# Kernel tuning notes

Measured on AMD Instinct MI355X. Metric: run time of the kernel, lower is better.

## Reference

```python
import jax, jax.numpy as jnp
import numpy as np

B, S, D, H = 2, 2048, 1024, 16
DK = D // H


def setup_inputs() -> dict:
    key = jax.random.key(0)
    ks = jax.random.split(key, 12)
    scale = 1.0 / np.sqrt(D)
    inp = {
        "Q": jax.random.normal(ks[0], (B, S, D), jnp.float32),
        "K": jax.random.normal(ks[1], (B, S, D), jnp.float32),
        "V": jax.random.normal(ks[2], (B, S, D), jnp.float32),
        # causal mask, broadcastable to [B, H, S, S]; 0 -> masked
        "Mask": jnp.tril(jnp.ones((S, S), jnp.int32))[None, None],
        "Wq": jax.random.normal(ks[3], (D, D), jnp.float32) * scale,
        "bq": jnp.zeros((D,), jnp.float32),
        "Wk": jax.random.normal(ks[4], (D, D), jnp.float32) * scale,
        "bk": jnp.zeros((D,), jnp.float32),
        "Wv": jax.random.normal(ks[5], (D, D), jnp.float32) * scale,
        "bv": jnp.zeros((D,), jnp.float32),
        "Wo": jax.random.normal(ks[6], (D, D), jnp.float32) * scale,
        "bo": jnp.zeros((D,), jnp.float32),
    }
    return inp


def _heads(x):
    # [B, S, D] -> [B, H, S, DK]
    return x.reshape(B, S, H, DK).transpose(0, 2, 1, 3)


def reference(Q, K, V, Mask, Wq, bq, Wk, bk, Wv, bv, Wo, bo):
    q = _heads(Q @ Wq.T + bq)
    k = _heads(K @ Wk.T + bk)
    v = _heads(V @ Wv.T + bv)
    # NOTE: original module does NOT scale by 1/sqrt(d_k)
    logits = jnp.einsum("bhqd,bhkd->bhqk", q, k)
    logits = jnp.where(Mask == 0, jnp.float32(-1e9), logits)
    attn = jax.nn.softmax(logits, axis=-1)  # dropout p=0.0 -> identity
    ctx = jnp.einsum("bhqk,bhkd->bhqd", attn, v)
    ctx = ctx.transpose(0, 2, 1, 3).reshape(B, S, D)
    return ctx @ Wo.T + bo
```

## Files before the change

kernel.cpp:

```cpp
#include <hip/hip_runtime.h>
#include <hip/hip_bf16.h>

#define B_  2
#define S_  2048
#define D_  1024
#define H_  16
#define DK_ 64
#define M_  (B_ * S_)

typedef __bf16 bf16;
typedef __bf16 bf16x8 __attribute__((ext_vector_type(8)));
typedef __bf16 bf16x4 __attribute__((ext_vector_type(4)));
typedef float  f32x4  __attribute__((ext_vector_type(4)));

#define MFMA16(a, b, c) __builtin_amdgcn_mfma_f32_16x16x32_bf16((a), (b), (c), 0, 0, 0)

__device__ __forceinline__ void gl2lds16(const bf16* g, bf16* l) {
    __builtin_amdgcn_global_load_lds((const __attribute__((address_space(1))) void*)g,
                                     (__attribute__((address_space(3))) void*)l, 16, 0, 0);
}

struct CastArgs { const float* src[7]; bf16* dst[7]; };

__global__ __launch_bounds__(256) void cast_all(CastArgs a) {
    int i = blockIdx.x * 256 + threadIdx.x;
    int seg, off;
    if (i < 3145728) { seg = i >> 20; off = i & 1048575; }
    else { int j = i - 3145728; seg = 3 + (j >> 18); off = j & 262143; }
    float4 v = ((const float4*)a.src[seg])[off];
    bf16x4 o;
    o[0] = (bf16)v.x; o[1] = (bf16)v.y; o[2] = (bf16)v.z; o[3] = (bf16)v.w;
    *(bf16x4*)&a.dst[seg][(size_t)off * 4] = o;
}

struct QkvArgs { const bf16* A[3]; const bf16* W[3]; const float* bias[3]; bf16* out[3]; };

__global__ __launch_bounds__(256, 3) void gemm_qkv(QkvArgs ar) {
    __shared__ bf16 As[128 * 32];
    __shared__ bf16 Bs[128 * 32];

    const int z = blockIdx.z;
    const bf16* A  = ar.A[z];
    const bf16* Bt = ar.W[z];
    const float* bias = ar.bias[z];
    bf16* Out = ar.out[z];
    const int mode = (z == 2) ? 1 : 0;

    const int t = threadIdx.x, lane = t & 63, w = t >> 6;
    const int lr = lane & 15, lq = lane >> 4;
    const int wm = (w >> 1) * 64, wn = (w & 1) * 64;
    const int n0 = blockIdx.x * 128, m0 = blockIdx.y * 128;

    const int c0 = w * 128 + lane, c1 = c0 + 64;
    const bf16* Ag0 = A  + (size_t)(m0 + (c0 >> 2)) * 1024 + (c0 & 3) * 8;
    const bf16* Ag1 = A  + (size_t)(m0 + (c1 >> 2)) * 1024 + (c1 & 3) * 8;
    const bf16* Bg0 = Bt + (size_t)(n0 + (c0 >> 2)) * 1024 + (c0 & 3) * 8;
    const bf16* Bg1 = Bt + (size_t)(n0 + (c1 >> 2)) * 1024 + (c1 & 3) * 8;
    bf16* Al0 = As + (w * 128) * 8;
    bf16* Al1 = As + (w * 128 + 64) * 8;
    bf16* Bl0 = Bs + (w * 128) * 8;
    bf16* Bl1 = Bs + (w * 128 + 64) * 8;

    f32x4 acc[4][4];
#pragma unroll
    for (int mi = 0; mi < 4; ++mi)
#pragma unroll
        for (int ni = 0; ni < 4; ++ni) acc[mi][ni] = 0.0f;

    for (int k0 = 0; k0 < 1024; k0 += 32) {
        __syncthreads();
        gl2lds16(Ag0 + k0, Al0);
        gl2lds16(Ag1 + k0, Al1);
        gl2lds16(Bg0 + k0, Bl0);
        gl2lds16(Bg1 + k0, Bl1);
        __syncthreads();
        bf16x8 af[4], bfr[4];
#pragma unroll
        for (int mi = 0; mi < 4; ++mi) af[mi]  = *(const bf16x8*)&As[(wm + mi * 16 + lr) * 32 + lq * 8];
#pragma unroll
        for (int ni = 0; ni < 4; ++ni) bfr[ni] = *(const bf16x8*)&Bs[(wn + ni * 16 + lr) * 32 + lq * 8];
#pragma unroll
        for (int mi = 0; mi < 4; ++mi)
#pragma unroll
            for (int ni = 0; ni < 4; ++ni) acc[mi][ni] = MFMA16(af[mi], bfr[ni], acc[mi][ni]);
    }

#pragma unroll
    for (int mi = 0; mi < 4; ++mi) {
#pragma unroll
        for (int ni = 0; ni < 4; ++ni) {
            int gn = n0 + wn + ni * 16 + lr;
            float bv = bias[gn];
#pragma unroll
            for (int r = 0; r < 4; ++r) {
                int gm = m0 + wm + mi * 16 + lq * 4 + r;
                float v = acc[mi][ni][r] + bv;
                int b = gm >> 11, s = gm & (S_ - 1);
                int h = gn >> 6, dk = gn & 63;
                if (mode == 0)
                    Out[(((size_t)(b * H_ + h) * S_ + s) << 6) + dk] = (bf16)v;
                else
                    Out[(((size_t)(b * H_ + h) * DK_ + dk) << 11) + s] = (bf16)v;
            }
        }
    }
}

__global__ __launch_bounds__(256, 2) void gemm_out(const bf16* __restrict__ A,
                                                   const bf16* __restrict__ Bt,
                                                   const float* __restrict__ bias,
                                                   float* __restrict__ Out) {
    __shared__ bf16 As[64 * 32];
    __shared__ bf16 Bs[128 * 32];

    const int t = threadIdx.x, lane = t & 63, w = t >> 6;
    const int lr = lane & 15, lq = lane >> 4;
    const int wm = (w >> 1) * 32, wn = (w & 1) * 64;
    const int n0 = blockIdx.x * 128, m0 = blockIdx.y * 64;

    const int ca = w * 64 + lane;
    const int cb0 = w * 128 + lane, cb1 = cb0 + 64;
    const bf16* Ag  = A  + (size_t)(m0 + (ca >> 2)) * 1024 + (ca & 3) * 8;
    const bf16* Bg0 = Bt + (size_t)(n0 + (cb0 >> 2)) * 1024 + (cb0 & 3) * 8;
    const bf16* Bg1 = Bt + (size_t)(n0 + (cb1 >> 2)) * 1024 + (cb1 & 3) * 8;
    bf16* Al  = As + (w * 64) * 8;
    bf16* Bl0 = Bs + (w * 128) * 8;
    bf16* Bl1 = Bs + (w * 128 + 64) * 8;

    f32x4 acc[2][4];
#pragma unroll
    for (int mi = 0; mi < 2; ++mi)
#pragma unroll
        for (int ni = 0; ni < 4; ++ni) acc[mi][ni] = 0.0f;

    for (int k0 = 0; k0 < 1024; k0 += 32) {
        __syncthreads();
        gl2lds16(Ag + k0, Al);
        gl2lds16(Bg0 + k0, Bl0);
        gl2lds16(Bg1 + k0, Bl1);
        __syncthreads();
        bf16x8 af[2], bfr[4];
#pragma unroll
        for (int mi = 0; mi < 2; ++mi) af[mi]  = *(const bf16x8*)&As[(wm + mi * 16 + lr) * 32 + lq * 8];
#pragma unroll
        for (int ni = 0; ni < 4; ++ni) bfr[ni] = *(const bf16x8*)&Bs[(wn + ni * 16 + lr) * 32 + lq * 8];
#pragma unroll
        for (int mi = 0; mi < 2; ++mi)
#pragma unroll
            for (int ni = 0; ni < 4; ++ni) acc[mi][ni] = MFMA16(af[mi], bfr[ni], acc[mi][ni]);
    }

#pragma unroll
    for (int mi = 0; mi < 2; ++mi) {
#pragma unroll
        for (int ni = 0; ni < 4; ++ni) {
            int gn = n0 + wn + ni * 16 + lr;
            float bv = bias[gn];
#pragma unroll
            for (int r = 0; r < 4; ++r) {
                int gm = m0 + wm + mi * 16 + lq * 4 + r;
                Out[(size_t)gm * 1024 + gn] = acc[mi][ni][r] + bv;
            }
        }
    }
}

__global__ __launch_bounds__(256, 2) void flash_attn(const bf16* __restrict__ qh,
                                                     const bf16* __restrict__ kh,
                                                     const bf16* __restrict__ vt,
                                                     bf16* __restrict__ ctx) {
    __shared__ char smem[40960];
    bf16* Qs = (bf16*)smem;
    bf16* Ks = (bf16*)(smem + 8192);
    bf16* Ps = (bf16*)(smem + 24576);

    const int pair = blockIdx.x, h = blockIdx.y, b = blockIdx.z;
    const int bh = b * H_ + h;
    const bf16* Qp = qh + (size_t)bh * S_ * DK_;
    const bf16* Kp = kh + (size_t)bh * S_ * DK_;
    const bf16* Vp = vt + (size_t)bh * DK_ * S_;

    const int t = threadIdx.x, lane = t & 63, w = t >> 6;
    const int lr = lane & 15, lq = lane >> 4;
    const int wq = w & 1, wk = w >> 1;
    bf16* Pw = Ps + w * 2048;

    for (int half = 0; half < 2; ++half) {
        const int qt = half ? (31 - pair) : pair;

#pragma unroll
        for (int i = 0; i < 2; ++i) {
            int c = w * 128 + i * 64 + lane;
            int qrow = c >> 3, xx = (c & 7) ^ (qrow & 7);
            gl2lds16(Qp + (size_t)(qt * 64 + qrow) * 64 + xx * 8, Qs + (w * 128 + i * 64) * 8);
        }

        f32x4 oacc[2][4];
#pragma unroll
        for (int mt = 0; mt < 2; ++mt)
#pragma unroll
            for (int nt = 0; nt < 4; ++nt) oacc[mt][nt] = 0.0f;
        float lpart[2] = {0.f, 0.f};

        const int nkt = qt / 2 + 1;
        for (int kt = 0; kt < nkt; ++kt) {
            __syncthreads();
#pragma unroll
            for (int i = 0; i < 4; ++i) {
                int c = w * 256 + i * 64 + lane;
                int krow = c >> 3, xx = (c & 7) ^ (krow & 7);
                gl2lds16(Kp + (size_t)(kt * 128 + krow) * 64 + xx * 8, Ks + (w * 256 + i * 64) * 8);
            }
            __syncthreads();

            const int k64 = kt * 2 + wk;
            if (k64 <= qt) {
                bf16x8 bv[2][4];
#pragma unroll
                for (int kk = 0; kk < 2; ++kk)
#pragma unroll
                    for (int nt = 0; nt < 4; ++nt)
                        bv[kk][nt] = *(const bf16x8*)(Vp + (size_t)(nt * 16 + lr) * S_ +
                                                      kt * 128 + wk * 64 + kk * 32 + lq * 8);
                f32x4 s[4][2];
#pragma unroll
                for (int mt = 0; mt < 4; ++mt)
#pragma unroll
                    for (int nt = 0; nt < 2; ++nt) s[mt][nt] = 0.0f;
#pragma unroll
                for (int ks = 0; ks < 2; ++ks) {
                    bf16x8 af[4], qf[2];
                    int xx = (ks * 4 + lq) ^ (lr & 7);
#pragma unroll
                    for (int mt = 0; mt < 4; ++mt)
                        af[mt] = *(const bf16x8*)&Ks[(wk * 64 + mt * 16 + lr) * 64 + xx * 8];
#pragma unroll
                    for (int nt = 0; nt < 2; ++nt)
                        qf[nt] = *(const bf16x8*)&Qs[(wq * 32 + nt * 16 + lr) * 64 + xx * 8];
#pragma unroll
                    for (int mt = 0; mt < 4; ++mt)
#pragma unroll
                        for (int nt = 0; nt < 2; ++nt) s[mt][nt] = MFMA16(af[mt], qf[nt], s[mt][nt]);
                }
                const bool diag = (k64 == qt);
#pragma unroll
                for (int mt = 0; mt < 4; ++mt)
#pragma unroll
                    for (int nt = 0; nt < 2; ++nt) {
                        bf16x4 pb;
#pragma unroll
                        for (int r = 0; r < 4; ++r) {
                            int kl = mt * 16 + lq * 4 + r;
                            int qlT = wq * 32 + nt * 16 + lr;
                            float p = (!diag || kl <= qlT) ? __expf(s[mt][nt][r]) : 0.0f;
                            bf16 p16 = (bf16)p;
                            lpart[nt] += (float)p16;
                            pb[r] = p16;
                        }
                        int xx = (2 * mt + (lq >> 1)) ^ (lr & 7);
                        *(bf16x4*)&Pw[(nt * 16 + lr) * 64 + xx * 8 + (lq & 1) * 4] = pb;
                    }
#pragma unroll
                for (int kk = 0; kk < 2; ++kk) {
                    bf16x8 ap[2];
                    int xx = (kk * 4 + lq) ^ (lr & 7);
#pragma unroll
                    for (int mt2 = 0; mt2 < 2; ++mt2)
                        ap[mt2] = *(const bf16x8*)&Pw[(mt2 * 16 + lr) * 64 + xx * 8];
#pragma unroll
                    for (int mt2 = 0; mt2 < 2; ++mt2)
#pragma unroll
                        for (int nt = 0; nt < 4; ++nt)
                            oacc[mt2][nt] = MFMA16(ap[mt2], bv[kk][nt], oacc[mt2][nt]);
                }
            }
        }

        __syncthreads();
#pragma unroll
        for (int nt = 0; nt < 2; ++nt) {
            lpart[nt] += __shfl_xor(lpart[nt], 16);
            lpart[nt] += __shfl_xor(lpart[nt], 32);
        }
        float* Op = (float*)(smem + 24576);
        float* Lh = (float*)smem;
        if (lq == 0)
#pragma unroll
            for (int nt = 0; nt < 2; ++nt) Lh[wk * 64 + wq * 32 + nt * 16 + lr] = lpart[nt];
        if (wk == 1) {
#pragma unroll
            for (int mt = 0; mt < 2; ++mt)
#pragma unroll
                for (int nt = 0; nt < 4; ++nt)
#pragma unroll
                    for (int r = 0; r < 4; ++r) {
                        int row = mt * 16 + lq * 4 + r, col = nt * 16 + lr;
                        int xx = (col >> 2) ^ (row & 15);
                        Op[wq * 2048 + row * 64 + xx * 4 + (col & 3)] = oacc[mt][nt][r];
                    }
        }
        __syncthreads();
        if (wk == 0) {
            float linv[2][4];
#pragma unroll
            for (int mt = 0; mt < 2; ++mt)
#pragma unroll
                for (int r = 0; r < 4; ++r) {
                    int qq = wq * 32 + mt * 16 + lq * 4 + r;
                    linv[mt][r] = 1.0f / (Lh[qq] + Lh[64 + qq]);
                }
#pragma unroll
            for (int mt = 0; mt < 2; ++mt)
#pragma unroll
                for (int nt = 0; nt < 4; ++nt)
#pragma unroll
                    for (int r = 0; r < 4; ++r) {
                        int row = mt * 16 + lq * 4 + r, col = nt * 16 + lr;
                        int xx = (col >> 2) ^ (row & 15);
                        float v = (oacc[mt][nt][r] + Op[wq * 2048 + row * 64 + xx * 4 + (col & 3)]) * linv[mt][r];
                        int q = qt * 64 + wq * 32 + row;
                        ctx[((size_t)(b * S_ + q)) * D_ + h * DK_ + col] = (bf16)v;
                    }
        }
        __syncthreads();
    }
}

extern "C" void kernel_launch(void* const* d_in, const int* in_sizes, int n_in,
                              void* d_out, int out_size, void* d_ws, size_t ws_size,
                              hipStream_t stream) {
    const float* Q  = (const float*)d_in[0];
    const float* K  = (const float*)d_in[1];
    const float* V  = (const float*)d_in[2];
    const float* Wq = (const float*)d_in[4];
    const float* bq = (const float*)d_in[5];
    const float* Wk = (const float*)d_in[6];
    const float* bk = (const float*)d_in[7];
    const float* Wv = (const float*)d_in[8];
    const float* bv = (const float*)d_in[9];
    const float* Wo = (const float*)d_in[10];
    const float* bo = (const float*)d_in[11];

    char* p = (char*)d_ws;
    bf16* Qb  = (bf16*)p;  p += (size_t)M_ * D_ * 2;
    bf16* Kb  = (bf16*)p;  p += (size_t)M_ * D_ * 2;
    bf16* Vb  = (bf16*)p;  p += (size_t)M_ * D_ * 2;
    bf16* Wqb = (bf16*)p;  p += (size_t)D_ * D_ * 2;
    bf16* Wkb = (bf16*)p;  p += (size_t)D_ * D_ * 2;
    bf16* Wvb = (bf16*)p;  p += (size_t)D_ * D_ * 2;
    bf16* Wob = (bf16*)p;  p += (size_t)D_ * D_ * 2;
    bf16* qhd = (bf16*)p;  p += (size_t)M_ * D_ * 2;
    bf16* khd = (bf16*)p;  p += (size_t)M_ * D_ * 2;
    bf16* vtr = (bf16*)p;  p += (size_t)M_ * D_ * 2;
    bf16* ctx = (bf16*)p;  p += (size_t)M_ * D_ * 2;

    CastArgs ca;
    ca.src[0] = Q;  ca.dst[0] = Qb;
    ca.src[1] = K;  ca.dst[1] = Kb;
    ca.src[2] = V;  ca.dst[2] = Vb;
    ca.src[3] = Wq; ca.dst[3] = Wqb;
    ca.src[4] = Wk; ca.dst[4] = Wkb;
    ca.src[5] = Wv; ca.dst[5] = Wvb;
    ca.src[6] = Wo; ca.dst[6] = Wob;
    cast_all<<<16384, 256, 0, stream>>>(ca);

    QkvArgs qa;
    qa.A[0] = Qb;  qa.A[1] = Kb;  qa.A[2] = Vb;
    qa.W[0] = Wqb; qa.W[1] = Wkb; qa.W[2] = Wvb;
    qa.bias[0] = bq; qa.bias[1] = bk; qa.bias[2] = bv;
    qa.out[0] = qhd; qa.out[1] = khd; qa.out[2] = vtr;
    dim3 qgrid(D_ / 128, M_ / 128, 3);
    gemm_qkv<<<qgrid, 256, 0, stream>>>(qa);

    dim3 fgrid(16, H_, B_);
    flash_attn<<<fgrid, 256, 0, stream>>>(qhd, khd, vtr, ctx);

    dim3 ogrid(D_ / 128, M_ / 64);
    gemm_out<<<ogrid, 256, 0, stream>>>(ctx, Wob, bo, (float*)d_out);
}
```

Before: 240.6 us.

## Shrink attention query tile to 32 rows and stage V-transpose stores through LDS

The flash attention kernel now processes 32-query tiles, with each of four waves handling a 32-key slice. This doubles the grid to 1024 blocks with a swizzled block-to-head mapping, cuts LDS use, and raises the occupancy hint to 4 blocks. The partial outputs and row sums of the four waves are reduced through LDS at the end. Separately, the QKV GEMM's transposed V output is staged in a padded LDS tile so it can be written with 16-byte coalesced stores instead of scattered 2-byte writes. The price is extra LDS traffic and a larger shared-memory footprint in the GEMM, which may lower its occupancy.

```diff
diff --git a/kernel.cpp b/kernel.cpp
--- a/kernel.cpp
+++ b/kernel.cpp
@@ -38,6 +38,7 @@
 __global__ __launch_bounds__(256, 3) void gemm_qkv(QkvArgs ar) {
     __shared__ bf16 As[128 * 32];
     __shared__ bf16 Bs[128 * 32];
+    __shared__ bf16 Cs[128 * 136];
 
     const int z = blockIdx.z;
     const bf16* A  = ar.A[z];
@@ -85,23 +86,45 @@
             for (int ni = 0; ni < 4; ++ni) acc[mi][ni] = MFMA16(af[mi], bfr[ni], acc[mi][ni]);
     }
 
-#pragma unroll
-    for (int mi = 0; mi < 4; ++mi) {
-#pragma unroll
-        for (int ni = 0; ni < 4; ++ni) {
-            int gn = n0 + wn + ni * 16 + lr;
-            float bv = bias[gn];
-#pragma unroll
-            for (int r = 0; r < 4; ++r) {
-                int gm = m0 + wm + mi * 16 + lq * 4 + r;
-                float v = acc[mi][ni][r] + bv;
-                int b = gm >> 11, s = gm & (S_ - 1);
-                int h = gn >> 6, dk = gn & 63;
-                if (mode == 0)
+    if (mode == 0) {
+#pragma unroll
+        for (int mi = 0; mi < 4; ++mi) {
+#pragma unroll
+            for (int ni = 0; ni < 4; ++ni) {
+                int gn = n0 + wn + ni * 16 + lr;
+                float bv = bias[gn];
+#pragma unroll
+                for (int r = 0; r < 4; ++r) {
+                    int gm = m0 + wm + mi * 16 + lq * 4 + r;
+                    float v = acc[mi][ni][r] + bv;
+                    int b = gm >> 11, s = gm & (S_ - 1);
+                    int h = gn >> 6, dk = gn & 63;
                     Out[(((size_t)(b * H_ + h) * S_ + s) << 6) + dk] = (bf16)v;
-                else
-                    Out[(((size_t)(b * H_ + h) * DK_ + dk) << 11) + s] = (bf16)v;
+                }
             }
+        }
+    } else {
+#pragma unroll
+        for (int mi = 0; mi < 4; ++mi) {
+#pragma unroll
+            for (int ni = 0; ni < 4; ++ni) {
+                int n = wn + ni * 16 + lr;
+                float bv = bias[n0 + n];
+                bf16x4 pk;
+#pragma unroll
+                for (int r = 0; r < 4; ++r) pk[r] = (bf16)(acc[mi][ni][r] + bv);
+                *(bf16x4*)&Cs[n * 136 + wm + mi * 16 + lq * 4] = pk;
+            }
+        }
+        __syncthreads();
+        const int b = m0 >> 11, s0 = m0 & (S_ - 1);
+#pragma unroll
+        for (int j = 0; j < 8; ++j) {
+            int cc = j * 256 + t;
+            int n = cc >> 4, cm = cc & 15;
+            int gn = n0 + n, h = gn >> 6, dk = gn & 63;
+            bf16x8 v = *(const bf16x8*)&Cs[n * 136 + cm * 8];
+            *(bf16x8*)&Out[(((size_t)(b * H_ + h) * DK_ + dk) << 11) + s0 + cm * 8] = v;
         }
     }
 }
@@ -165,34 +188,35 @@
     }
 }
 
-__global__ __launch_bounds__(256, 2) void flash_attn(const bf16* __restrict__ qh,
+__global__ __launch_bounds__(256, 4) void flash_attn(const bf16* __restrict__ qh,
                                                      const bf16* __restrict__ kh,
                                                      const bf16* __restrict__ vt,
                                                      bf16* __restrict__ ctx) {
-    __shared__ char smem[40960];
+    __shared__ char smem[30720];
     bf16* Qs = (bf16*)smem;
-    bf16* Ks = (bf16*)(smem + 8192);
-    bf16* Ps = (bf16*)(smem + 24576);
-
-    const int pair = blockIdx.x, h = blockIdx.y, b = blockIdx.z;
-    const int bh = b * H_ + h;
+    bf16* Ks = (bf16*)(smem + 4096);
+    bf16* Ps = (bf16*)(smem + 20480);
+
+    const int id = blockIdx.x;
+    const int bh = (id & 7) * 4 + ((id >> 3) & 3);
+    const int pr = id >> 5;
+    const int b = bh >> 4, h = bh & 15;
+
     const bf16* Qp = qh + (size_t)bh * S_ * DK_;
     const bf16* Kp = kh + (size_t)bh * S_ * DK_;
     const bf16* Vp = vt + (size_t)bh * DK_ * S_;
 
     const int t = threadIdx.x, lane = t & 63, w = t >> 6;
     const int lr = lane & 15, lq = lane >> 4;
-    const int wq = w & 1, wk = w >> 1;
-    bf16* Pw = Ps + w * 2048;
+    bf16* Pw = Ps + w * (32 * 40);
 
     for (int half = 0; half < 2; ++half) {
-        const int qt = half ? (31 - pair) : pair;
-
-#pragma unroll
-        for (int i = 0; i < 2; ++i) {
-            int c = w * 128 + i * 64 + lane;
+        const int qt = half ? (63 - pr) : pr;
+
+        {
+            int c = w * 64 + lane;
             int qrow = c >> 3, xx = (c & 7) ^ (qrow & 7);
-            gl2lds16(Qp + (size_t)(qt * 64 + qrow) * 64 + xx * 8, Qs + (w * 128 + i * 64) * 8);
+            gl2lds16(Qp + (size_t)(qt * 32 + qrow) * 64 + xx * 8, Qs + (w * 64) * 8);
         }
 
         f32x4 oacc[2][4];
@@ -202,7 +226,7 @@
             for (int nt = 0; nt < 4; ++nt) oacc[mt][nt] = 0.0f;
         float lpart[2] = {0.f, 0.f};
 
-        const int nkt = qt / 2 + 1;
+        const int nkt = (qt >> 2) + 1;
         for (int kt = 0; kt < nkt; ++kt) {
             __syncthreads();
 #pragma unroll
@@ -213,66 +237,64 @@
             }
             __syncthreads();
 
-            const int k64 = kt * 2 + wk;
-            if (k64 <= qt) {
-                bf16x8 bv[2][4];
-#pragma unroll
-                for (int kk = 0; kk < 2; ++kk)
-#pragma unroll
-                    for (int nt = 0; nt < 4; ++nt)
-                        bv[kk][nt] = *(const bf16x8*)(Vp + (size_t)(nt * 16 + lr) * S_ +
-                                                      kt * 128 + wk * 64 + kk * 32 + lq * 8);
-                f32x4 s[4][2];
-#pragma unroll
-                for (int mt = 0; mt < 4; ++mt)
+            const int k32 = kt * 4 + w;
+            if (k32 <= qt) {
+                bf16x8 bv[4];
+#pragma unroll
+                for (int nt = 0; nt < 4; ++nt)
+                    bv[nt] = *(const bf16x8*)(Vp + (size_t)(nt * 16 + lr) * S_ +
+                                              kt * 128 + w * 32 + lq * 8);
+                f32x4 s[2][2];
+#pragma unroll
+                for (int mt = 0; mt < 2; ++mt)
 #pragma unroll
                     for (int nt = 0; nt < 2; ++nt) s[mt][nt] = 0.0f;
 #pragma unroll
                 for (int ks = 0; ks < 2; ++ks) {
-                    bf16x8 af[4], qf[2];
-                    int xx = (ks * 4 + lq) ^ (lr & 7);
-#pragma unroll
-                    for (int mt = 0; mt < 4; ++mt)
-                        af[mt] = *(const bf16x8*)&Ks[(wk * 64 + mt * 16 + lr) * 64 + xx * 8];
-#pragma unroll
-                    for (int nt = 0; nt < 2; ++nt)
-                        qf[nt] = *(const bf16x8*)&Qs[(wq * 32 + nt * 16 + lr) * 64 + xx * 8];
-#pragma unroll
-                    for (int mt = 0; mt < 4; ++mt)
+                    bf16x8 af[2], qf[2];
+#pragma unroll
+                    for (int mt = 0; mt < 2; ++mt) {
+                        int krow = w * 32 + mt * 16 + lr;
+                        int xx = (ks * 4 + lq) ^ (krow & 7);
+                        af[mt] = *(const bf16x8*)&Ks[krow * 64 + xx * 8];
+                    }
+#pragma unroll
+                    for (int nt = 0; nt < 2; ++nt) {
+                        int q = nt * 16 + lr;
+                        int xx = (ks * 4 + lq) ^ (q & 7);
+                        qf[nt] = *(const bf16x8*)&Qs[q * 64 + xx * 8];
+                    }
+#pragma unroll
+                    for (int mt = 0; mt < 2; ++mt)
 #pragma unroll
                         for (int nt = 0; nt < 2; ++nt) s[mt][nt] = MFMA16(af[mt], qf[nt], s[mt][nt]);
                 }
-                const bool diag = (k64 == qt);
-#pragma unroll
-                for (int mt = 0; mt < 4; ++mt)
+                const bool diag = (k32 == qt);
+#pragma unroll
+                for (int mt = 0; mt < 2; ++mt)
 #pragma unroll
                     for (int nt = 0; nt < 2; ++nt) {
                         bf16x4 pb;
 #pragma unroll
                         for (int r = 0; r < 4; ++r) {
                             int kl = mt * 16 + lq * 4 + r;
-                            int qlT = wq * 32 + nt * 16 + lr;
-                            float p = (!diag || kl <= qlT) ? __expf(s[mt][nt][r]) : 0.0f;
+                            int ql = nt * 16 + lr;
+                            float p = (!diag || kl <= ql) ? __expf(s[mt][nt][r]) : 0.0f;
                             bf16 p16 = (bf16)p;
                             lpart[nt] += (float)p16;
                             pb[r] = p16;
                         }
-                        int xx = (2 * mt + (lq >> 1)) ^ (lr & 7);
-                        *(bf16x4*)&Pw[(nt * 16 + lr) * 64 + xx * 8 + (lq & 1) * 4] = pb;
+                        *(bf16x4*)&Pw[(nt * 16 + lr) * 40 + mt * 16 + lq * 4] = pb;
                     }
-#pragma unroll
-                for (int kk = 0; kk < 2; ++kk) {
-                    bf16x8 ap[2];
-                    int xx = (kk * 4 + lq) ^ (lr & 7);
-#pragma unroll
-                    for (int mt2 = 0; mt2 < 2; ++mt2)
-                        ap[mt2] = *(const bf16x8*)&Pw[(mt2 * 16 + lr) * 64 + xx * 8];
-#pragma unroll
-                    for (int mt2 = 0; mt2 < 2; ++mt2)
-#pragma unroll
-                        for (int nt = 0; nt < 4; ++nt)
-                            oacc[mt2][nt] = MFMA16(ap[mt2], bv[kk][nt], oacc[mt2][nt]);
-                }
+                bf16x8 ap[2];
+#pragma unroll
+                for (int mt2 = 0; mt2 < 2; ++mt2)
+                    ap[mt2] = *(const bf16x8*)&Pw[(mt2 * 16 + lr) * 40 + lq * 8];
+#pragma unroll
+                for (int mt2 = 0; mt2 < 2; ++mt2)
+#pragma unroll
+                    for (int nt = 0; nt < 4; ++nt)
+                        oacc[mt2][nt] = MFMA16(ap[mt2], bv[nt], oacc[mt2][nt]);
             }
         }
 
@@ -282,32 +304,31 @@
             lpart[nt] += __shfl_xor(lpart[nt], 16);
             lpart[nt] += __shfl_xor(lpart[nt], 32);
         }
-        float* Op = (float*)(smem + 24576);
-        float* Lh = (float*)smem;
+        float* Op = (float*)smem;
+        float* Lh = (float*)(smem + 26112);
         if (lq == 0)
 #pragma unroll
-            for (int nt = 0; nt < 2; ++nt) Lh[wk * 64 + wq * 32 + nt * 16 + lr] = lpart[nt];
-        if (wk == 1) {
+            for (int nt = 0; nt < 2; ++nt) Lh[w * 32 + nt * 16 + lr] = lpart[nt];
+        if (w > 0) {
 #pragma unroll
             for (int mt = 0; mt < 2; ++mt)
 #pragma unroll
                 for (int nt = 0; nt < 4; ++nt)
 #pragma unroll
                     for (int r = 0; r < 4; ++r) {
-                        int row = mt * 16 + lq * 4 + r, col = nt * 16 + lr;
-                        int xx = (col >> 2) ^ (row & 15);
-                        Op[wq * 2048 + row * 64 + xx * 4 + (col & 3)] = oacc[mt][nt][r];
+                        int q = mt * 16 + lq * 4 + r, dk = nt * 16 + lr;
+                        Op[(w - 1) * 2176 + q * 68 + dk] = oacc[mt][nt][r];
                     }
         }
         __syncthreads();
-        if (wk == 0) {
+        if (w == 0) {
             float linv[2][4];
 #pragma unroll
             for (int mt = 0; mt < 2; ++mt)
 #pragma unroll
                 for (int r = 0; r < 4; ++r) {
-                    int qq = wq * 32 + mt * 16 + lq * 4 + r;
-                    linv[mt][r] = 1.0f / (Lh[qq] + Lh[64 + qq]);
+                    int q = mt * 16 + lq * 4 + r;
+                    linv[mt][r] = 1.0f / (Lh[q] + Lh[32 + q] + Lh[64 + q] + Lh[96 + q]);
                 }
 #pragma unroll
             for (int mt = 0; mt < 2; ++mt)
@@ -315,11 +336,12 @@
                 for (int nt = 0; nt < 4; ++nt)
 #pragma unroll
                     for (int r = 0; r < 4; ++r) {
-                        int row = mt * 16 + lq * 4 + r, col = nt * 16 + lr;
-                        int xx = (col >> 2) ^ (row & 15);
-                        float v = (oacc[mt][nt][r] + Op[wq * 2048 + row * 64 + xx * 4 + (col & 3)]) * linv[mt][r];
-                        int q = qt * 64 + wq * 32 + row;
-                        ctx[((size_t)(b * S_ + q)) * D_ + h * DK_ + col] = (bf16)v;
+                        int q = mt * 16 + lq * 4 + r, dk = nt * 16 + lr;
+                        float v = oacc[mt][nt][r] + Op[q * 68 + dk]
+                                + Op[2176 + q * 68 + dk] + Op[4352 + q * 68 + dk];
+                        v *= linv[mt][r];
+                        int qg = qt * 32 + q;
+                        ctx[((size_t)(b * S_ + qg)) * D_ + h * DK_ + dk] = (bf16)v;
                     }
         }
         __syncthreads();
@@ -372,8 +394,7 @@
     dim3 qgrid(D_ / 128, M_ / 128, 3);
     gemm_qkv<<<qgrid, 256, 0, stream>>>(qa);
 
-    dim3 fgrid(16, H_, B_);
-    flash_attn<<<fgrid, 256, 0, stream>>>(qhd, khd, vtr, ctx);
+    flash_attn<<<1024, 256, 0, stream>>>(qhd, khd, vtr, ctx);
 
     dim3 ogrid(D_ / 128, M_ / 64);
     gemm_out<<<ogrid, 256, 0, stream>>>(ctx, Wob, bo, (float*)d_out);
```

New measurement: 241.6 us. Within noise of the previous version (+0.4%).

## Deepen GEMM K-tiles with swizzled LDS, stage V-transpose store, remap attention blocks to XCDs

Applied to the files above, without the earlier changes.

Both projection GEMMs now load a 64-wide K slice per iteration into XOR-swizzled LDS tiles, halving the number of barrier pairs and avoiding bank conflicts on fragment reads. The transposed V output goes through an LDS staging buffer so global stores become contiguous 16-byte writes instead of scattered 2-byte writes. Flash attention uses a 1D grid whose block index is remapped so that all blocks for a given batch-head land on the same XCD, improving L2 reuse of K/V. Larger LDS footprints may reduce occupancy.

```diff
diff --git a/kernel.cpp b/kernel.cpp
--- a/kernel.cpp
+++ b/kernel.cpp
@@ -36,8 +36,10 @@
 struct QkvArgs { const bf16* A[3]; const bf16* W[3]; const float* bias[3]; bf16* out[3]; };
 
 __global__ __launch_bounds__(256, 3) void gemm_qkv(QkvArgs ar) {
-    __shared__ bf16 As[128 * 32];
-    __shared__ bf16 Bs[128 * 32];
+    __shared__ char smem[34816];
+    bf16* As = (bf16*)smem;
+    bf16* Bs = (bf16*)(smem + 16384);
+    bf16* Cs = (bf16*)smem;
 
     const int z = blockIdx.z;
     const bf16* A  = ar.A[z];
@@ -51,15 +53,16 @@
     const int wm = (w >> 1) * 64, wn = (w & 1) * 64;
     const int n0 = blockIdx.x * 128, m0 = blockIdx.y * 128;
 
-    const int c0 = w * 128 + lane, c1 = c0 + 64;
-    const bf16* Ag0 = A  + (size_t)(m0 + (c0 >> 2)) * 1024 + (c0 & 3) * 8;
-    const bf16* Ag1 = A  + (size_t)(m0 + (c1 >> 2)) * 1024 + (c1 & 3) * 8;
-    const bf16* Bg0 = Bt + (size_t)(n0 + (c0 >> 2)) * 1024 + (c0 & 3) * 8;
-    const bf16* Bg1 = Bt + (size_t)(n0 + (c1 >> 2)) * 1024 + (c1 & 3) * 8;
-    bf16* Al0 = As + (w * 128) * 8;
-    bf16* Al1 = As + (w * 128 + 64) * 8;
-    bf16* Bl0 = Bs + (w * 128) * 8;
-    bf16* Bl1 = Bs + (w * 128 + 64) * 8;
+    const bf16* Ag[4]; const bf16* Bg[4]; bf16* Al[4]; bf16* Bl[4];
+#pragma unroll
+    for (int i = 0; i < 4; ++i) {
+        int c = i * 256 + w * 64 + lane;
+        int row = c >> 3, x = (c & 7) ^ (row & 7);
+        Ag[i] = A  + (size_t)(m0 + row) * 1024 + x * 8;
+        Bg[i] = Bt + (size_t)(n0 + row) * 1024 + x * 8;
+        Al[i] = As + (i * 256 + w * 64) * 8;
+        Bl[i] = Bs + (i * 256 + w * 64) * 8;
+    }
 
     f32x4 acc[4][4];
 #pragma unroll
@@ -67,41 +70,74 @@
 #pragma unroll
         for (int ni = 0; ni < 4; ++ni) acc[mi][ni] = 0.0f;
 
-    for (int k0 = 0; k0 < 1024; k0 += 32) {
-        __syncthreads();
-        gl2lds16(Ag0 + k0, Al0);
-        gl2lds16(Ag1 + k0, Al1);
-        gl2lds16(Bg0 + k0, Bl0);
-        gl2lds16(Bg1 + k0, Bl1);
-        __syncthreads();
-        bf16x8 af[4], bfr[4];
-#pragma unroll
-        for (int mi = 0; mi < 4; ++mi) af[mi]  = *(const bf16x8*)&As[(wm + mi * 16 + lr) * 32 + lq * 8];
-#pragma unroll
-        for (int ni = 0; ni < 4; ++ni) bfr[ni] = *(const bf16x8*)&Bs[(wn + ni * 16 + lr) * 32 + lq * 8];
-#pragma unroll
-        for (int mi = 0; mi < 4; ++mi)
-#pragma unroll
-            for (int ni = 0; ni < 4; ++ni) acc[mi][ni] = MFMA16(af[mi], bfr[ni], acc[mi][ni]);
-    }
-
-#pragma unroll
-    for (int mi = 0; mi < 4; ++mi) {
-#pragma unroll
-        for (int ni = 0; ni < 4; ++ni) {
-            int gn = n0 + wn + ni * 16 + lr;
-            float bv = bias[gn];
-#pragma unroll
-            for (int r = 0; r < 4; ++r) {
-                int gm = m0 + wm + mi * 16 + lq * 4 + r;
-                float v = acc[mi][ni][r] + bv;
-                int b = gm >> 11, s = gm & (S_ - 1);
-                int h = gn >> 6, dk = gn & 63;
-                if (mode == 0)
+    for (int k0 = 0; k0 < 1024; k0 += 64) {
+        __syncthreads();
+#pragma unroll
+        for (int i = 0; i < 4; ++i) {
+            gl2lds16(Ag[i] + k0, Al[i]);
+            gl2lds16(Bg[i] + k0, Bl[i]);
+        }
+        __syncthreads();
+#pragma unroll
+        for (int ks = 0; ks < 2; ++ks) {
+            bf16x8 af[4], bfr[4];
+#pragma unroll
+            for (int mi = 0; mi < 4; ++mi) {
+                int row = wm + mi * 16 + lr;
+                af[mi] = *(const bf16x8*)&As[row * 64 + ((ks * 4 + lq) ^ (row & 7)) * 8];
+            }
+#pragma unroll
+            for (int ni = 0; ni < 4; ++ni) {
+                int row = wn + ni * 16 + lr;
+                bfr[ni] = *(const bf16x8*)&Bs[row * 64 + ((ks * 4 + lq) ^ (row & 7)) * 8];
+            }
+#pragma unroll
+            for (int mi = 0; mi < 4; ++mi)
+#pragma unroll
+                for (int ni = 0; ni < 4; ++ni) acc[mi][ni] = MFMA16(af[mi], bfr[ni], acc[mi][ni]);
+        }
+    }
+
+    if (mode == 0) {
+#pragma unroll
+        for (int mi = 0; mi < 4; ++mi) {
+#pragma unroll
+            for (int ni = 0; ni < 4; ++ni) {
+                int gn = n0 + wn + ni * 16 + lr;
+                float bv = bias[gn];
+#pragma unroll
+                for (int r = 0; r < 4; ++r) {
+                    int gm = m0 + wm + mi * 16 + lq * 4 + r;
+                    float v = acc[mi][ni][r] + bv;
+                    int b = gm >> 11, s = gm & (S_ - 1);
+                    int h = gn >> 6, dk = gn & 63;
                     Out[(((size_t)(b * H_ + h) * S_ + s) << 6) + dk] = (bf16)v;
-                else
-                    Out[(((size_t)(b * H_ + h) * DK_ + dk) << 11) + s] = (bf16)v;
-            }
+                }
+            }
+        }
+    } else {
+        __syncthreads();
+#pragma unroll
+        for (int mi = 0; mi < 4; ++mi) {
+#pragma unroll
+            for (int ni = 0; ni < 4; ++ni) {
+                int n = wn + ni * 16 + lr;
+                float bv = bias[n0 + n];
+                bf16x4 pk;
+#pragma unroll
+                for (int r = 0; r < 4; ++r) pk[r] = (bf16)(acc[mi][ni][r] + bv);
+                *(bf16x4*)&Cs[n * 136 + wm + mi * 16 + lq * 4] = pk;
+            }
+        }
+        __syncthreads();
+        const int b = m0 >> 11, s0 = m0 & (S_ - 1);
+#pragma unroll
+        for (int j = 0; j < 8; ++j) {
+            int cc = j * 256 + t;
+            int n = cc >> 4, cm = cc & 15;
+            int gn = n0 + n, h = gn >> 6, dk = gn & 63;
+            bf16x8 v = *(const bf16x8*)&Cs[n * 136 + cm * 8];
+            *(bf16x8*)&Out[(((size_t)(b * H_ + h) * DK_ + dk) << 11) + s0 + cm * 8] = v;
         }
     }
 }
@@ -110,22 +146,30 @@
                                                    const bf16* __restrict__ Bt,
                                                    const float* __restrict__ bias,
                                                    float* __restrict__ Out) {
-    __shared__ bf16 As[64 * 32];
-    __shared__ bf16 Bs[128 * 32];
+    __shared__ bf16 As[64 * 64];
+    __shared__ bf16 Bs[128 * 64];
 
     const int t = threadIdx.x, lane = t & 63, w = t >> 6;
     const int lr = lane & 15, lq = lane >> 4;
     const int wm = (w >> 1) * 32, wn = (w & 1) * 64;
     const int n0 = blockIdx.x * 128, m0 = blockIdx.y * 64;
 
-    const int ca = w * 64 + lane;
-    const int cb0 = w * 128 + lane, cb1 = cb0 + 64;
-    const bf16* Ag  = A  + (size_t)(m0 + (ca >> 2)) * 1024 + (ca & 3) * 8;
-    const bf16* Bg0 = Bt + (size_t)(n0 + (cb0 >> 2)) * 1024 + (cb0 & 3) * 8;
-    const bf16* Bg1 = Bt + (size_t)(n0 + (cb1 >> 2)) * 1024 + (cb1 & 3) * 8;
-    bf16* Al  = As + (w * 64) * 8;
-    bf16* Bl0 = Bs + (w * 128) * 8;
-    bf16* Bl1 = Bs + (w * 128 + 64) * 8;
+    const bf16* Ag[2]; bf16* Al[2];
+#pragma unroll
+    for (int i = 0; i < 2; ++i) {
+        int c = i * 256 + w * 64 + lane;
+        int row = c >> 3, x = (c & 7) ^ (row & 7);
+        Ag[i] = A + (size_t)(m0 + row) * 1024 + x * 8;
+        Al[i] = As + (i * 256 + w * 64) * 8;
+    }
+    const bf16* Bg[4]; bf16* Bl[4];
+#pragma unroll
+    for (int i = 0; i < 4; ++i) {
+        int c = i * 256 + w * 64 + lane;
+        int row = c >> 3, x = (c & 7) ^ (row & 7);
+        Bg[i] = Bt + (size_t)(n0 + row) * 1024 + x * 8;
+        Bl[i] = Bs + (i * 256 + w * 64) * 8;
+    }
 
     f32x4 acc[2][4];
 #pragma unroll
@@ -133,21 +177,31 @@
 #pragma unroll
         for (int ni = 0; ni < 4; ++ni) acc[mi][ni] = 0.0f;
 
-    for (int k0 = 0; k0 < 1024; k0 += 32) {
-        __syncthreads();
-        gl2lds16(Ag + k0, Al);
-        gl2lds16(Bg0 + k0, Bl0);
-        gl2lds16(Bg1 + k0, Bl1);
-        __syncthreads();
-        bf16x8 af[2], bfr[4];
-#pragma unroll
-        for (int mi = 0; mi < 2; ++mi) af[mi]  = *(const bf16x8*)&As[(wm + mi * 16 + lr) * 32 + lq * 8];
-#pragma unroll
-        for (int ni = 0; ni < 4; ++ni) bfr[ni] = *(const bf16x8*)&Bs[(wn + ni * 16 + lr) * 32 + lq * 8];
-#pragma unroll
-        for (int mi = 0; mi < 2; ++mi)
-#pragma unroll
-            for (int ni = 0; ni < 4; ++ni) acc[mi][ni] = MFMA16(af[mi], bfr[ni], acc[mi][ni]);
+    for (int k0 = 0; k0 < 1024; k0 += 64) {
+        __syncthreads();
+#pragma unroll
+        for (int i = 0; i < 2; ++i) gl2lds16(Ag[i] + k0, Al[i]);
+#pragma unroll
+        for (int i = 0; i < 4; ++i) gl2lds16(Bg[i] + k0, Bl[i]);
+        __syncthreads();
+#pragma unroll
+        for (int ks = 0; ks < 2; ++ks) {
+            bf16x8 af[2], bfr[4];
+#pragma unroll
+            for (int mi = 0; mi < 2; ++mi) {
+                int row = wm + mi * 16 + lr;
+                af[mi] = *(const bf16x8*)&As[row * 64 + ((ks * 4 + lq) ^ (row & 7)) * 8];
+            }
+#pragma unroll
+            for (int ni = 0; ni < 4; ++ni) {
+                int row = wn + ni * 16 + lr;
+                bfr[ni] = *(const bf16x8*)&Bs[row * 64 + ((ks * 4 + lq) ^ (row & 7)) * 8];
+            }
+#pragma unroll
+            for (int mi = 0; mi < 2; ++mi)
+#pragma unroll
+                for (int ni = 0; ni < 4; ++ni) acc[mi][ni] = MFMA16(af[mi], bfr[ni], acc[mi][ni]);
+        }
     }
 
 #pragma unroll
@@ -174,8 +228,12 @@
     bf16* Ks = (bf16*)(smem + 8192);
     bf16* Ps = (bf16*)(smem + 24576);
 
-    const int pair = blockIdx.x, h = blockIdx.y, b = blockIdx.z;
-    const int bh = b * H_ + h;
+    const int id = blockIdx.x;
+    const int xcd = id & 7, loc = id >> 3;
+    const int bh = xcd * 4 + (loc & 3);
+    const int pair = loc >> 2;
+    const int b = bh >> 4, h = bh & 15;
+
     const bf16* Qp = qh + (size_t)bh * S_ * DK_;
     const bf16* Kp = kh + (size_t)bh * S_ * DK_;
     const bf16* Vp = vt + (size_t)bh * DK_ * S_;
@@ -372,8 +430,7 @@
     dim3 qgrid(D_ / 128, M_ / 128, 3);
     gemm_qkv<<<qgrid, 256, 0, stream>>>(qa);
 
-    dim3 fgrid(16, H_, B_);
-    flash_attn<<<fgrid, 256, 0, stream>>>(qhd, khd, vtr, ctx);
+    flash_attn<<<512, 256, 0, stream>>>(qhd, khd, vtr, ctx);
 
     dim3 ogrid(D_ / 128, M_ / 64);
     gemm_out<<<ogrid, 256, 0, stream>>>(ctx, Wob, bo, (float*)d_out);
```

Measured after the change: 223.2 us. 7.2% less time.
